# Kernel tuning notes

Hardware: AMD Instinct MI355X
Metric: run time of the kernel (lower is better)

## Reference

```python
import jax, jax.numpy as jnp
import numpy as np

N_NODES = 100000
N_EDGES = 1600000
NUM_GRAPHS = 256


def _gcn_conv(x, src, dst, deg_isqrt, deg_inv, W, b):
    # GCNConv with self-loops and symmetric normalization (PyG semantics):
    # out_i = sum_{j->i} d_j^-1/2 d_i^-1/2 (x_j W) + d_i^-1 (x_i W) + b
    xl = x @ W  # [N, out]
    norm = deg_isqrt[src] * deg_isqrt[dst]  # [E]
    msgs = norm[:, None] * xl[src]  # [E, out] -- dominant memory traffic
    agg = jax.ops.segment_sum(msgs, dst, num_segments=N_NODES)
    return agg + deg_inv[:, None] * xl + b


def setup_inputs() -> dict:
    key = jax.random.key(0)
    ks = jax.random.split(key, 8)
    F_in, H, T = 128, 128, 64
    x = jax.random.normal(ks[0], (N_NODES, F_in), dtype=jnp.float32)
    edge_index = jax.random.randint(ks[1], (2, N_EDGES), 0, N_NODES, dtype=jnp.int64)
    batch = jnp.sort(jax.random.randint(ks[2], (N_NODES,), 0, NUM_GRAPHS, dtype=jnp.int64))
    s0 = 1.0 / np.sqrt(F_in)
    s1 = 1.0 / np.sqrt(H)
    return {
        "x": x,
        "edge_index": edge_index,
        "batch": batch,
        "W0": jax.random.normal(ks[3], (F_in, H), dtype=jnp.float32) * s0,
        "b0": jnp.zeros((H,), dtype=jnp.float32),
        "W1": jax.random.normal(ks[4], (H, H), dtype=jnp.float32) * s1,
        "b1": jnp.zeros((H,), dtype=jnp.float32),
        "W2": jax.random.normal(ks[5], (H, T), dtype=jnp.float32) * s1,
        "b2": jnp.zeros((T,), dtype=jnp.float32),
    }


def reference(x, edge_index, batch, W0, b0, W1, b1, W2, b2):
    src, dst = edge_index[0], edge_index[1]
    # degree including self-loop
    deg = jax.ops.segment_sum(jnp.ones((N_EDGES,), x.dtype), dst, num_segments=N_NODES) + 1.0
    deg_isqrt = jax.lax.rsqrt(deg)
    deg_inv = 1.0 / deg

    h = jax.nn.gelu(_gcn_conv(x, src, dst, deg_isqrt, deg_inv, W0, b0))
    h = jax.nn.gelu(_gcn_conv(h, src, dst, deg_isqrt, deg_inv, W1, b1))
    h = jax.nn.gelu(_gcn_conv(h, src, dst, deg_isqrt, deg_inv, W2, b2))

    # global_mean_pool over graphs
    sums = jax.ops.segment_sum(h, batch, num_segments=NUM_GRAPHS)
    counts = jax.ops.segment_sum(jnp.ones((N_NODES,), h.dtype), batch, num_segments=NUM_GRAPHS)
    return sums / jnp.maximum(counts, 1.0)[:, None]
```

## Files before the change

### kernel.cpp

```cpp
#include <hip/hip_runtime.h>
#include <math.h>

#define F_IN 128
#define TDIM 64
#define NGRAPH 256

typedef __attribute__((ext_vector_type(8))) short short8;
typedef __attribute__((ext_vector_type(4))) float f32x4;

__device__ __forceinline__ float gelu_f(float x) {
    float x3 = x * x * x;
    return 0.5f * x * (1.0f + tanhf(0.7978845608028654f * (x + 0.044715f * x3)));
}

__device__ __forceinline__ unsigned short bf16_of(float x) {
    unsigned u = __float_as_uint(x);
    return (unsigned short)((u + 0x7fffu + ((u >> 16) & 1u)) >> 16);
}
__device__ __forceinline__ float f_of(unsigned short h) {
    return __uint_as_float(((unsigned)h) << 16);
}
__device__ __forceinline__ unsigned bf16pair(float a, float b) {
    return (unsigned)bf16_of(a) | ((unsigned)bf16_of(b) << 16);
}
__device__ __forceinline__ float2 bf16unpack(unsigned u) {
    float2 r;
    r.x = __uint_as_float(u << 16);
    r.y = __uint_as_float(u & 0xffff0000u);
    return r;
}


#define BIN_CH 4096
#define MAXNB 512
#define CAP 6144

__global__ __launch_bounds__(256) void binC_kernel(const int* __restrict__ src,
                                                   const int* __restrict__ dst,
                                                   int* __restrict__ bucket_cnt,
                                                   unsigned* __restrict__ tmp, int E, int NB) {
    __shared__ int hist[MAXNB];
    __shared__ int hbase[MAXNB];
    __shared__ int hcur[MAXNB];
    int tid = threadIdx.x;
    int base = blockIdx.x * BIN_CH;
    int end = base + BIN_CH;
    if (end > E) end = E;
    for (int i = tid; i < NB; i += 256) hist[i] = 0;
    __syncthreads();
    for (int e = base + tid; e < end; e += 256) atomicAdd(&hist[dst[e] >> 8], 1);
    __syncthreads();
    for (int i = tid; i < NB; i += 256) {
        int c = hist[i];
        hbase[i] = (c > 0) ? atomicAdd(&bucket_cnt[i], c) : 0;
        hcur[i] = 0;
    }
    __syncthreads();
    for (int e = base + tid; e < end; e += 256) {
        int d = dst[e];
        int b = d >> 8;
        int p = atomicAdd(&hcur[b], 1);
        int slot = hbase[b] + p;
        if (slot < CAP)
            tmp[(size_t)b * CAP + slot] = (unsigned)src[e] | ((unsigned)(d & 255) << 24);
    }
}

__global__ void scanBuckets_kernel(const int* __restrict__ bucket_cnt,
                                   int* __restrict__ bbase, int* __restrict__ row_off,
                                   int NB, int N) {
    if (threadIdx.x == 0 && blockIdx.x == 0) {
        int c = 0;
        for (int i = 0; i < NB; ++i) {
            bbase[i] = c;
            int v = bucket_cnt[i];
            c += (v < CAP ? v : CAP);
        }
        row_off[N] = c;
    }
}

__global__ __launch_bounds__(256) void binDcount_kernel(const unsigned* __restrict__ tmp,
                                                        const int* __restrict__ bucket_cnt,
                                                        const int* __restrict__ bbase,
                                                        int* __restrict__ row_off,
                                                        float* __restrict__ isq,
                                                        float* __restrict__ dinv, int N) {
    __shared__ int lcnt[256];
    __shared__ int sh[256];
    int b = blockIdx.x;
    int tid = threadIdx.x;
    int cntb = bucket_cnt[b];
    if (cntb > CAP) cntb = CAP;
    lcnt[tid] = 0;
    __syncthreads();
    const unsigned* tb = tmp + (size_t)b * CAP;
    for (int e = tid; e < cntb; e += 256) atomicAdd(&lcnt[tb[e] >> 24], 1);
    __syncthreads();
    int own = lcnt[tid];
    sh[tid] = own;
    __syncthreads();
    for (int off = 1; off < 256; off <<= 1) {
        int x = (tid >= off) ? sh[tid - off] : 0;
        __syncthreads();
        sh[tid] += x;
        __syncthreads();
    }
    int excl = sh[tid] - own;
    int node = (b << 8) + tid;
    if (node < N) {
        row_off[node] = bbase[b] + excl;
        float d = (float)own + 1.0f;
        isq[node] = rsqrtf(d);
        dinv[node] = 1.0f / d;
    }
}

__global__ __launch_bounds__(256) void binDscatter_kernel(const unsigned* __restrict__ tmp,
                                                          const int* __restrict__ bucket_cnt,
                                                          const int* __restrict__ row_off,
                                                          const float* __restrict__ isq,
                                                          uint2* __restrict__ edges, int N) {
    __shared__ int lcur[256];
    __shared__ float lisq[256];
    int b = blockIdx.x;
    int node0 = b << 8;
    int tid = threadIdx.x;
    lcur[tid] = 0;
    int nd = node0 + tid;
    lisq[tid] = (nd < N) ? isq[nd] : 0.f;
    __syncthreads();
    int cntb = bucket_cnt[b];
    if (cntb > CAP) cntb = CAP;
    const unsigned* tb = tmp + (size_t)b * CAP;
    for (int e = tid; e < cntb; e += 256) {
        unsigned rec = tb[e];
        int dl = (int)(rec >> 24);
        unsigned s = rec & 0xFFFFFFu;
        int p = atomicAdd(&lcur[dl], 1);
        float nrm = isq[s] * lisq[dl];
        edges[(size_t)row_off[node0 + dl] + p] = make_uint2(s, __float_as_uint(nrm));
    }
}


__global__ __launch_bounds__(256) void wconv_all_kernel(const float* __restrict__ W0,
                                                        const float* __restrict__ W1,
                                                        const float* __restrict__ W2,
                                                        unsigned short* __restrict__ hi0,
                                                        unsigned short* __restrict__ lo0,
                                                        unsigned short* __restrict__ hi1,
                                                        unsigned short* __restrict__ lo1,
                                                        unsigned short* __restrict__ hi2,
                                                        unsigned short* __restrict__ lo2) {
    int idx = blockIdx.x * blockDim.x + threadIdx.x;
    const float* W;
    unsigned short *whi, *wlo;
    int local, FOUT;
    if (idx < 16384) {
        W = W0; whi = hi0; wlo = lo0; local = idx; FOUT = 128;
    } else if (idx < 32768) {
        W = W1; whi = hi1; wlo = lo1; local = idx - 16384; FOUT = 128;
    } else if (idx < 40960) {
        W = W2; whi = hi2; wlo = lo2; local = idx - 32768; FOUT = 64;
    } else {
        return;
    }
    int k = local / FOUT;
    int n = local % FOUT;
    float w = W[local];
    unsigned short h = bf16_of(w);
    whi[(size_t)n * 128 + k] = h;
    wlo[(size_t)n * 128 + k] = bf16_of(w - f_of(h));
}


#define LROW 136

template <int FOUT>
__global__ __launch_bounds__(256) void gemm_mfma_kernel(const float* __restrict__ X,
                                                        const unsigned short* __restrict__ whiT,
                                                        const unsigned short* __restrict__ wloT,
                                                        unsigned* __restrict__ Yb, int nrows) {
    constexpr int NT = FOUT / 16;
    __shared__ short lds[2 * FOUT * LROW];
    short* shi = lds;
    short* slo = lds + FOUT * LROW;

    for (int c = threadIdx.x; c < FOUT * 16; c += 256) {
        int n = c >> 4, r = c & 15;
        *(short8*)(shi + n * LROW + r * 8) = *(const short8*)(whiT + (size_t)n * 128 + r * 8);
        *(short8*)(slo + n * LROW + r * 8) = *(const short8*)(wloT + (size_t)n * 128 + r * 8);
    }
    __syncthreads();

    int lane = threadIdx.x & 63;
    int wave = threadIdx.x >> 6;
    int quad = lane >> 4;
    int l16 = lane & 15;
    int rowBase = blockIdx.x * 128 + wave * 32;

    f32x4 acc[2][NT];
#pragma unroll
    for (int m = 0; m < 2; ++m)
#pragma unroll
        for (int t = 0; t < NT; ++t) acc[m][t] = (f32x4){0.f, 0.f, 0.f, 0.f};

    int arow0 = rowBase + l16;
    int arow1 = rowBase + 16 + l16;
    bool ok0 = arow0 < nrows, ok1 = arow1 < nrows;
    const float* xr0 = X + (size_t)arow0 * 128;
    const float* xr1 = X + (size_t)arow1 * 128;

#pragma unroll
    for (int k0 = 0; k0 < 128; k0 += 32) {
        short8 ahi[2], alo[2];
#pragma unroll
        for (int m = 0; m < 2; ++m) {
            const float* xr = m ? xr1 : xr0;
            bool ok = m ? ok1 : ok0;
            float xv[8];
            if (ok) {
                float4 v0 = *(const float4*)(xr + k0 + quad * 8);
                float4 v1 = *(const float4*)(xr + k0 + quad * 8 + 4);
                xv[0] = v0.x; xv[1] = v0.y; xv[2] = v0.z; xv[3] = v0.w;
                xv[4] = v1.x; xv[5] = v1.y; xv[6] = v1.z; xv[7] = v1.w;
            } else {
#pragma unroll
                for (int j = 0; j < 8; ++j) xv[j] = 0.f;
            }
#pragma unroll
            for (int j = 0; j < 8; ++j) {
                unsigned short h = bf16_of(xv[j]);
                ahi[m][j] = (short)h;
                alo[m][j] = (short)bf16_of(xv[j] - f_of(h));
            }
        }
#pragma unroll
        for (int t = 0; t < NT; ++t) {
            int off = (t * 16 + l16) * LROW + k0 + quad * 8;
            short8 bhi = *(const short8*)(shi + off);
            short8 blo = *(const short8*)(slo + off);
#pragma unroll
            for (int m = 0; m < 2; ++m) {
                acc[m][t] = __builtin_amdgcn_mfma_f32_16x16x32_bf16(ahi[m], bhi, acc[m][t], 0, 0, 0);
                acc[m][t] = __builtin_amdgcn_mfma_f32_16x16x32_bf16(alo[m], bhi, acc[m][t], 0, 0, 0);
                acc[m][t] = __builtin_amdgcn_mfma_f32_16x16x32_bf16(ahi[m], blo, acc[m][t], 0, 0, 0);
            }
        }
    }

#pragma unroll
    for (int m = 0; m < 2; ++m) {
#pragma unroll
        for (int t = 0; t < NT; ++t) {
            int col = t * 16 + l16;
#pragma unroll
            for (int i = 0; i < 4; ++i) {
                int r = rowBase + m * 16 + quad * 4 + i;
                float v = acc[m][t][i];
                float nb = __shfl_xor(v, 1, 64);
                if (((lane & 1) == 0) && r < nrows)
                    Yb[(size_t)r * (FOUT / 2) + (col >> 1)] = bf16pair(v, nb);
            }
        }
    }
}


__global__ __launch_bounds__(256) void agg128_kernel(const unsigned* __restrict__ xlb,
                                                     const int* __restrict__ row_off,
                                                     const uint2* __restrict__ edges,
                                                     const float* __restrict__ dinv,
                                                     const float* __restrict__ bias,
                                                     float* __restrict__ out, int nnodes) {
    int wave = (blockIdx.x * blockDim.x + threadIdx.x) >> 6;
    int lane = threadIdx.x & 63;
    if (wave >= nnodes) return;
    int e0 = __builtin_amdgcn_readfirstlane(row_off[wave]);
    int e1 = __builtin_amdgcn_readfirstlane(row_off[wave + 1]);
    float ax = 0.f, ay = 0.f;
    int rounds = (e1 - e0 + 15) >> 4;
    for (int r = 0; r < rounds; ++r) {
        int base = e0 + (r << 4);
        int idx = base + (lane & 15);
        int cl = idx < e1 ? idx : e1 - 1;
        uint2 edv = edges[cl];
        unsigned sx[16];
        float nw[16];
#pragma unroll
        for (int j = 0; j < 16; ++j) {
            sx[j] = (unsigned)__builtin_amdgcn_readlane((int)edv.x, j);
            unsigned ny = (unsigned)__builtin_amdgcn_readlane((int)edv.y, j);
            nw[j] = (base + j < e1) ? __uint_as_float(ny) : 0.f;
        }
        unsigned v[16];
#pragma unroll
        for (int j = 0; j < 16; ++j) v[j] = xlb[(size_t)sx[j] * 64 + lane];
#pragma unroll
        for (int j = 0; j < 16; ++j) {
            float2 f = bf16unpack(v[j]);
            ax += nw[j] * f.x;
            ay += nw[j] * f.y;
        }
    }
    float di = dinv[wave];
    float2 pi = bf16unpack(xlb[(size_t)wave * 64 + lane]);
    float2 bb = *(const float2*)(bias + lane * 2);
    float2 o;
    o.x = gelu_f(ax + di * pi.x + bb.x);
    o.y = gelu_f(ay + di * pi.y + bb.y);
    *(float2*)(out + (size_t)wave * 128 + lane * 2) = o;
}


__global__ __launch_bounds__(256) void agg64_kernel(const unsigned* __restrict__ xlb,
                                                    const int* __restrict__ row_off,
                                                    const uint2* __restrict__ edges,
                                                    const float* __restrict__ dinv,
                                                    const float* __restrict__ bias,
                                                    float* __restrict__ out, int nnodes) {
    int wave = (blockIdx.x * blockDim.x + threadIdx.x) >> 6;
    int lane = threadIdx.x & 63;
    int sub = lane >> 5;
    int sl = lane & 31;
    int node = wave * 2 + sub;
    bool nv = node < nnodes;
    int e0 = nv ? row_off[node] : 0;
    int e1 = nv ? row_off[node + 1] : 0;
    int rounds = (e1 - e0 + 15) >> 4;
    int ro = __shfl_xor(rounds, 32, 64);
    int maxr = rounds > ro ? rounds : ro;
    float ax = 0.f, ay = 0.f;
    for (int r = 0; r < maxr; ++r) {
        int base = e0 + (r << 4);
        uint2 ed[16];
#pragma unroll
        for (int j = 0; j < 16; ++j) {
            int idx = base + j;
            int cl = idx < e1 ? idx : (e1 > e0 ? e1 - 1 : 0);
            ed[j] = edges[cl];
            if (idx >= e1) ed[j].y = 0u;
        }
        unsigned v[16];
#pragma unroll
        for (int j = 0; j < 16; ++j) v[j] = xlb[(size_t)ed[j].x * 32 + sl];
#pragma unroll
        for (int j = 0; j < 16; ++j) {
            float nw = __uint_as_float(ed[j].y);
            float2 f = bf16unpack(v[j]);
            ax += nw * f.x;
            ay += nw * f.y;
        }
    }
    if (nv) {
        float di = dinv[node];
        float2 pi = bf16unpack(xlb[(size_t)node * 32 + sl]);
        float2 bb = *(const float2*)(bias + sl * 2);
        float2 o;
        o.x = gelu_f(ax + di * pi.x + bb.x);
        o.y = gelu_f(ay + di * pi.y + bb.y);
        *(float2*)(out + (size_t)node * 64 + sl * 2) = o;
    }
}


#define POOL_CHUNK 64

__global__ __launch_bounds__(256) void pool_kernel(const float* __restrict__ h,
                                                   const int* __restrict__ batch,
                                                   float* __restrict__ psum,
                                                   float* __restrict__ pcnt, int nnodes) {
    int wave = (blockIdx.x * blockDim.x + threadIdx.x) >> 6;
    int lane = threadIdx.x & 63;
    int n0 = wave * POOL_CHUNK;
    if (n0 >= nnodes) return;
    int n1 = n0 + POOL_CHUNK;
    if (n1 > nnodes) n1 = nnodes;

    int g_cur = batch[n0];
    float acc = 0.f;
    int cnt = 0;
    for (int node = n0; node < n1; ++node) {
        int g = batch[node];
        if (g != g_cur) {
            atomicAdd(&psum[g_cur * TDIM + lane], acc);
            if (lane == 0) atomicAdd(&pcnt[g_cur], (float)cnt);
            acc = 0.f;
            cnt = 0;
            g_cur = g;
        }
        acc += h[(size_t)node * TDIM + lane];
        ++cnt;
    }
    atomicAdd(&psum[g_cur * TDIM + lane], acc);
    if (lane == 0) atomicAdd(&pcnt[g_cur], (float)cnt);
}

__global__ __launch_bounds__(256) void fin_kernel(const float* __restrict__ psum,
                                                  const float* __restrict__ pcnt,
                                                  float* __restrict__ out) {
    int i = blockIdx.x * blockDim.x + threadIdx.x;
    if (i < NGRAPH * TDIM) {
        float c = pcnt[i >> 6];
        out[i] = psum[i] / fmaxf(c, 1.0f);
    }
}


extern "C" void kernel_launch(void* const* d_in, const int* in_sizes, int n_in,
                              void* d_out, int out_size, void* d_ws, size_t ws_size,
                              hipStream_t stream) {
    const float* x = (const float*)d_in[0];
    const int* ei = (const int*)d_in[1];
    const int* batch = (const int*)d_in[2];
    const float* W0 = (const float*)d_in[3];
    const float* b0 = (const float*)d_in[4];
    const float* W1 = (const float*)d_in[5];
    const float* b1 = (const float*)d_in[6];
    const float* W2 = (const float*)d_in[7];
    const float* b2 = (const float*)d_in[8];

    const int N = in_sizes[0] / F_IN;
    const int E = in_sizes[1] / 2;
    const int* src = ei;
    const int* dst = ei + E;
    const int NB = (N + 255) >> 8;

    char* w = (char*)d_ws;
    auto alloc = [&](size_t bytes) -> void* {
        void* p = (void*)w;
        w += (bytes + 255) & ~(size_t)255;
        return p;
    };
    float* isq = (float*)alloc((size_t)N * 4);
    float* dinv = (float*)alloc((size_t)N * 4);
    int* bucket_cnt = (int*)alloc((size_t)MAXNB * 4);
    int* bbase = (int*)alloc((size_t)MAXNB * 4);
    int* row_off = (int*)alloc((size_t)(N + 1) * 4);
    uint2* edges = (uint2*)alloc((size_t)E * 8);
    unsigned* tmp = (unsigned*)alloc((size_t)NB * CAP * 4);
    float* psum = (float*)alloc((size_t)NGRAPH * TDIM * 4);
    float* pcnt = (float*)alloc((size_t)NGRAPH * 4);
    float* bufH = (float*)alloc((size_t)N * 128 * 4);
    unsigned* bufXb = (unsigned*)alloc((size_t)N * 64 * 4);
    unsigned short* whiT0 = (unsigned short*)alloc(128 * 128 * 2);
    unsigned short* wloT0 = (unsigned short*)alloc(128 * 128 * 2);
    unsigned short* whiT1 = (unsigned short*)alloc(128 * 128 * 2);
    unsigned short* wloT1 = (unsigned short*)alloc(128 * 128 * 2);
    unsigned short* whiT2 = (unsigned short*)alloc(64 * 128 * 2);
    unsigned short* wloT2 = (unsigned short*)alloc(64 * 128 * 2);

    hipMemsetAsync(bucket_cnt, 0, (size_t)MAXNB * 4, stream);
    hipMemsetAsync(psum, 0, (size_t)NGRAPH * TDIM * 4, stream);
    hipMemsetAsync(pcnt, 0, (size_t)NGRAPH * 4, stream);

    int cblocks = (E + BIN_CH - 1) / BIN_CH;
    binC_kernel<<<cblocks, 256, 0, stream>>>(src, dst, bucket_cnt, tmp, E, NB);
    scanBuckets_kernel<<<1, 64, 0, stream>>>(bucket_cnt, bbase, row_off, NB, N);
    binDcount_kernel<<<NB, 256, 0, stream>>>(tmp, bucket_cnt, bbase, row_off, isq, dinv, N);
    binDscatter_kernel<<<NB, 256, 0, stream>>>(tmp, bucket_cnt, row_off, isq, edges, N);

    wconv_all_kernel<<<(40960 + 255) / 256, 256, 0, stream>>>(W0, W1, W2, whiT0, wloT0, whiT1,
                                                              wloT1, whiT2, wloT2);

    int gblocks = (N + 127) / 128;
    int ablocks = (N * 64 + 255) / 256;
    int a64blocks = (((N + 1) / 2) * 64 + 255) / 256;

    gemm_mfma_kernel<128><<<gblocks, 256, 0, stream>>>(x, whiT0, wloT0, bufXb, N);
    agg128_kernel<<<ablocks, 256, 0, stream>>>(bufXb, row_off, edges, dinv, b0, bufH, N);
    gemm_mfma_kernel<128><<<gblocks, 256, 0, stream>>>(bufH, whiT1, wloT1, bufXb, N);
    agg128_kernel<<<ablocks, 256, 0, stream>>>(bufXb, row_off, edges, dinv, b1, bufH, N);
    gemm_mfma_kernel<64><<<gblocks, 256, 0, stream>>>(bufH, whiT2, wloT2, bufXb, N);
    agg64_kernel<<<a64blocks, 256, 0, stream>>>(bufXb, row_off, edges, dinv, b2, bufH, N);

    int pwaves = (N + POOL_CHUNK - 1) / POOL_CHUNK;
    int pblocks = (pwaves * 64 + 255) / 256;
    pool_kernel<<<pblocks, 256, 0, stream>>>(bufH, batch, psum, pcnt, N);
    fin_kernel<<<(NGRAPH * TDIM + 255) / 256, 256, 0, stream>>>(psum, pcnt, (float*)d_out);
}
```

Baseline: 458.6 us.

## Store hidden activations in bf16 and merge scan with weight conversion

The aggregation kernels now write post-GELU activations as packed bf16 instead of fp32. The layer-2/3 GEMMs read those bf16 activations directly as single MFMA A operands, and the pooling kernel unpacks bf16. The goal is to halve activation write/read traffic between layers and to drop one kernel launch by folding weight conversion into the bucket scan kernel. In exchange, intermediate activations lose precision, since only the hi/lo split of the weights is kept.

```diff
diff --git a/kernel.cpp b/kernel.cpp
--- a/kernel.cpp
+++ b/kernel.cpp
@@ -66,18 +66,49 @@
     }
 }
 
-__global__ void scanBuckets_kernel(const int* __restrict__ bucket_cnt,
-                                   int* __restrict__ bbase, int* __restrict__ row_off,
-                                   int NB, int N) {
-    if (threadIdx.x == 0 && blockIdx.x == 0) {
-        int c = 0;
-        for (int i = 0; i < NB; ++i) {
-            bbase[i] = c;
-            int v = bucket_cnt[i];
-            c += (v < CAP ? v : CAP);
-        }
-        row_off[N] = c;
-    }
+__global__ __launch_bounds__(256) void scan_wconv_kernel(const int* __restrict__ bucket_cnt,
+                                                         int* __restrict__ bbase,
+                                                         int* __restrict__ row_off, int NB,
+                                                         int N, const float* __restrict__ W0,
+                                                         const float* __restrict__ W1,
+                                                         const float* __restrict__ W2,
+                                                         unsigned short* __restrict__ hi0,
+                                                         unsigned short* __restrict__ lo0,
+                                                         unsigned short* __restrict__ hi1,
+                                                         unsigned short* __restrict__ lo1,
+                                                         unsigned short* __restrict__ hi2,
+                                                         unsigned short* __restrict__ lo2) {
+    if (blockIdx.x == 0) {
+        if (threadIdx.x == 0) {
+            int c = 0;
+            for (int i = 0; i < NB; ++i) {
+                bbase[i] = c;
+                int v = bucket_cnt[i];
+                c += (v < CAP ? v : CAP);
+            }
+            row_off[N] = c;
+        }
+        return;
+    }
+    int idx = (blockIdx.x - 1) * 256 + threadIdx.x;
+    const float* W;
+    unsigned short *whi, *wlo;
+    int local, FOUT;
+    if (idx < 16384) {
+        W = W0; whi = hi0; wlo = lo0; local = idx; FOUT = 128;
+    } else if (idx < 32768) {
+        W = W1; whi = hi1; wlo = lo1; local = idx - 16384; FOUT = 128;
+    } else if (idx < 40960) {
+        W = W2; whi = hi2; wlo = lo2; local = idx - 32768; FOUT = 64;
+    } else {
+        return;
+    }
+    int k = local / FOUT;
+    int n = local % FOUT;
+    float w = W[local];
+    unsigned short h = bf16_of(w);
+    whi[(size_t)n * 128 + k] = h;
+    wlo[(size_t)n * 128 + k] = bf16_of(w - f_of(h));
 }
 
 __global__ __launch_bounds__(256) void binDcount_kernel(const unsigned* __restrict__ tmp,
@@ -144,44 +175,13 @@
 }
 
 
-__global__ __launch_bounds__(256) void wconv_all_kernel(const float* __restrict__ W0,
-                                                        const float* __restrict__ W1,
-                                                        const float* __restrict__ W2,
-                                                        unsigned short* __restrict__ hi0,
-                                                        unsigned short* __restrict__ lo0,
-                                                        unsigned short* __restrict__ hi1,
-                                                        unsigned short* __restrict__ lo1,
-                                                        unsigned short* __restrict__ hi2,
-                                                        unsigned short* __restrict__ lo2) {
-    int idx = blockIdx.x * blockDim.x + threadIdx.x;
-    const float* W;
-    unsigned short *whi, *wlo;
-    int local, FOUT;
-    if (idx < 16384) {
-        W = W0; whi = hi0; wlo = lo0; local = idx; FOUT = 128;
-    } else if (idx < 32768) {
-        W = W1; whi = hi1; wlo = lo1; local = idx - 16384; FOUT = 128;
-    } else if (idx < 40960) {
-        W = W2; whi = hi2; wlo = lo2; local = idx - 32768; FOUT = 64;
-    } else {
-        return;
-    }
-    int k = local / FOUT;
-    int n = local % FOUT;
-    float w = W[local];
-    unsigned short h = bf16_of(w);
-    whi[(size_t)n * 128 + k] = h;
-    wlo[(size_t)n * 128 + k] = bf16_of(w - f_of(h));
-}
-
-
 #define LROW 136
 
-template <int FOUT>
-__global__ __launch_bounds__(256) void gemm_mfma_kernel(const float* __restrict__ X,
-                                                        const unsigned short* __restrict__ whiT,
-                                                        const unsigned short* __restrict__ wloT,
-                                                        unsigned* __restrict__ Yb, int nrows) {
+__global__ __launch_bounds__(256) void gemm_f32_kernel(const float* __restrict__ X,
+                                                       const unsigned short* __restrict__ whiT,
+                                                       const unsigned short* __restrict__ wloT,
+                                                       unsigned* __restrict__ Yb, int nrows) {
+    constexpr int FOUT = 128;
     constexpr int NT = FOUT / 16;
     __shared__ short lds[2 * FOUT * LROW];
     short* shi = lds;
@@ -268,12 +268,90 @@
 }
 
 
+template <int FOUT>
+__global__ __launch_bounds__(256) void gemm_bf16_kernel(const unsigned* __restrict__ Xb,
+                                                        const unsigned short* __restrict__ whiT,
+                                                        const unsigned short* __restrict__ wloT,
+                                                        unsigned* __restrict__ Yb, int nrows) {
+    constexpr int NT = FOUT / 16;
+    __shared__ short lds[2 * FOUT * LROW];
+    short* shi = lds;
+    short* slo = lds + FOUT * LROW;
+
+    for (int c = threadIdx.x; c < FOUT * 16; c += 256) {
+        int n = c >> 4, r = c & 15;
+        *(short8*)(shi + n * LROW + r * 8) = *(const short8*)(whiT + (size_t)n * 128 + r * 8);
+        *(short8*)(slo + n * LROW + r * 8) = *(const short8*)(wloT + (size_t)n * 128 + r * 8);
+    }
+    __syncthreads();
+
+    int lane = threadIdx.x & 63;
+    int wave = threadIdx.x >> 6;
+    int quad = lane >> 4;
+    int l16 = lane & 15;
+    int rowBase = blockIdx.x * 128 + wave * 32;
+
+    f32x4 acc[2][NT];
+#pragma unroll
+    for (int m = 0; m < 2; ++m)
+#pragma unroll
+        for (int t = 0; t < NT; ++t) acc[m][t] = (f32x4){0.f, 0.f, 0.f, 0.f};
+
+    int arow0 = rowBase + l16;
+    int arow1 = rowBase + 16 + l16;
+    bool ok0 = arow0 < nrows, ok1 = arow1 < nrows;
+    const short* xs0 = (const short*)Xb + (size_t)arow0 * 128;
+    const short* xs1 = (const short*)Xb + (size_t)arow1 * 128;
+
+#pragma unroll
+    for (int k0 = 0; k0 < 128; k0 += 32) {
+        short8 a[2];
+#pragma unroll
+        for (int m = 0; m < 2; ++m) {
+            const short* xs = m ? xs1 : xs0;
+            bool ok = m ? ok1 : ok0;
+            if (ok)
+                a[m] = *(const short8*)(xs + k0 + quad * 8);
+            else
+                a[m] = (short8){0, 0, 0, 0, 0, 0, 0, 0};
+        }
+#pragma unroll
+        for (int t = 0; t < NT; ++t) {
+            int off = (t * 16 + l16) * LROW + k0 + quad * 8;
+            short8 bhi = *(const short8*)(shi + off);
+            short8 blo = *(const short8*)(slo + off);
+#pragma unroll
+            for (int m = 0; m < 2; ++m) {
+                acc[m][t] = __builtin_amdgcn_mfma_f32_16x16x32_bf16(a[m], bhi, acc[m][t], 0, 0, 0);
+                acc[m][t] = __builtin_amdgcn_mfma_f32_16x16x32_bf16(a[m], blo, acc[m][t], 0, 0, 0);
+            }
+        }
+    }
+
+#pragma unroll
+    for (int m = 0; m < 2; ++m) {
+#pragma unroll
+        for (int t = 0; t < NT; ++t) {
+            int col = t * 16 + l16;
+#pragma unroll
+            for (int i = 0; i < 4; ++i) {
+                int r = rowBase + m * 16 + quad * 4 + i;
+                float v = acc[m][t][i];
+                float nb = __shfl_xor(v, 1, 64);
+                if (((lane & 1) == 0) && r < nrows)
+                    Yb[(size_t)r * (FOUT / 2) + (col >> 1)] = bf16pair(v, nb);
+            }
+        }
+    }
+}
+
+
 __global__ __launch_bounds__(256) void agg128_kernel(const unsigned* __restrict__ xlb,
                                                      const int* __restrict__ row_off,
                                                      const uint2* __restrict__ edges,
                                                      const float* __restrict__ dinv,
                                                      const float* __restrict__ bias,
-                                                     float* __restrict__ out, int nnodes) {
+                                                     unsigned* __restrict__ outb, int nnodes) {
     int wave = (blockIdx.x * blockDim.x + threadIdx.x) >> 6;
     int lane = threadIdx.x & 63;
     if (wave >= nnodes) return;
@@ -307,10 +385,8 @@
     float di = dinv[wave];
     float2 pi = bf16unpack(xlb[(size_t)wave * 64 + lane]);
     float2 bb = *(const float2*)(bias + lane * 2);
-    float2 o;
-    o.x = gelu_f(ax + di * pi.x + bb.x);
-    o.y = gelu_f(ay + di * pi.y + bb.y);
-    *(float2*)(out + (size_t)wave * 128 + lane * 2) = o;
+    outb[(size_t)wave * 64 + lane] =
+        bf16pair(gelu_f(ax + di * pi.x + bb.x), gelu_f(ay + di * pi.y + bb.y));
 }
 
 
@@ -319,7 +395,7 @@
                                                     const uint2* __restrict__ edges,
                                                     const float* __restrict__ dinv,
                                                     const float* __restrict__ bias,
-                                                    float* __restrict__ out, int nnodes) {
+                                                    unsigned* __restrict__ outb, int nnodes) {
     int wave = (blockIdx.x * blockDim.x + threadIdx.x) >> 6;
     int lane = threadIdx.x & 63;
     int sub = lane >> 5;
@@ -357,44 +433,49 @@
         float di = dinv[node];
         float2 pi = bf16unpack(xlb[(size_t)node * 32 + sl]);
         float2 bb = *(const float2*)(bias + sl * 2);
-        float2 o;
-        o.x = gelu_f(ax + di * pi.x + bb.x);
-        o.y = gelu_f(ay + di * pi.y + bb.y);
-        *(float2*)(out + (size_t)node * 64 + sl * 2) = o;
+        outb[(size_t)node * 32 + sl] =
+            bf16pair(gelu_f(ax + di * pi.x + bb.x), gelu_f(ay + di * pi.y + bb.y));
     }
 }
 
 
 #define POOL_CHUNK 64
 
-__global__ __launch_bounds__(256) void pool_kernel(const float* __restrict__ h,
+__global__ __launch_bounds__(256) void pool_kernel(const unsigned* __restrict__ hb,
                                                    const int* __restrict__ batch,
                                                    float* __restrict__ psum,
                                                    float* __restrict__ pcnt, int nnodes) {
     int wave = (blockIdx.x * blockDim.x + threadIdx.x) >> 6;
     int lane = threadIdx.x & 63;
-    int n0 = wave * POOL_CHUNK;
+    int half = lane >> 5;
+    int p = lane & 31;
+    int n0 = wave * POOL_CHUNK + half * 32;
     if (n0 >= nnodes) return;
-    int n1 = n0 + POOL_CHUNK;
+    int n1 = n0 + 32;
     if (n1 > nnodes) n1 = nnodes;
 
     int g_cur = batch[n0];
-    float acc = 0.f;
+    float accx = 0.f, accy = 0.f;
     int cnt = 0;
     for (int node = n0; node < n1; ++node) {
         int g = batch[node];
         if (g != g_cur) {
-            atomicAdd(&psum[g_cur * TDIM + lane], acc);
-            if (lane == 0) atomicAdd(&pcnt[g_cur], (float)cnt);
-            acc = 0.f;
+            atomicAdd(&psum[g_cur * TDIM + 2 * p], accx);
+            atomicAdd(&psum[g_cur * TDIM + 2 * p + 1], accy);
+            if (p == 0) atomicAdd(&pcnt[g_cur], (float)cnt);
+            accx = 0.f;
+            accy = 0.f;
             cnt = 0;
             g_cur = g;
         }
-        acc += h[(size_t)node * TDIM + lane];
+        float2 f = bf16unpack(hb[(size_t)node * 32 + p]);
+        accx += f.x;
+        accy += f.y;
         ++cnt;
     }
-    atomicAdd(&psum[g_cur * TDIM + lane], acc);
-    if (lane == 0) atomicAdd(&pcnt[g_cur], (float)cnt);
+    atomicAdd(&psum[g_cur * TDIM + 2 * p], accx);
+    atomicAdd(&psum[g_cur * TDIM + 2 * p + 1], accy);
+    if (p == 0) atomicAdd(&pcnt[g_cur], (float)cnt);
 }
 
 __global__ __launch_bounds__(256) void fin_kernel(const float* __restrict__ psum,
@@ -442,8 +523,8 @@
     unsigned* tmp = (unsigned*)alloc((size_t)NB * CAP * 4);
     float* psum = (float*)alloc((size_t)NGRAPH * TDIM * 4);
     float* pcnt = (float*)alloc((size_t)NGRAPH * 4);
-    float* bufH = (float*)alloc((size_t)N * 128 * 4);
     unsigned* bufXb = (unsigned*)alloc((size_t)N * 64 * 4);
+    unsigned* bufHb = (unsigned*)alloc((size_t)N * 64 * 4);
     unsigned short* whiT0 = (unsigned short*)alloc(128 * 128 * 2);
     unsigned short* wloT0 = (unsigned short*)alloc(128 * 128 * 2);
     unsigned short* whiT1 = (unsigned short*)alloc(128 * 128 * 2);
@@ -457,26 +538,25 @@
 
     int cblocks = (E + BIN_CH - 1) / BIN_CH;
     binC_kernel<<<cblocks, 256, 0, stream>>>(src, dst, bucket_cnt, tmp, E, NB);
-    scanBuckets_kernel<<<1, 64, 0, stream>>>(bucket_cnt, bbase, row_off, NB, N);
+    scan_wconv_kernel<<<1 + (40960 + 255) / 256, 256, 0, stream>>>(
+        bucket_cnt, bbase, row_off, NB, N, W0, W1, W2, whiT0, wloT0, whiT1, wloT1, whiT2,
+        wloT2);
     binDcount_kernel<<<NB, 256, 0, stream>>>(tmp, bucket_cnt, bbase, row_off, isq, dinv, N);
     binDscatter_kernel<<<NB, 256, 0, stream>>>(tmp, bucket_cnt, row_off, isq, edges, N);
-
-    wconv_all_kernel<<<(40960 + 255) / 256, 256, 0, stream>>>(W0, W1, W2, whiT0, wloT0, whiT1,
-                                                              wloT1, whiT2, wloT2);
 
     int gblocks = (N + 127) / 128;
     int ablocks = (N * 64 + 255) / 256;
     int a64blocks = (((N + 1) / 2) * 64 + 255) / 256;
 
-    gemm_mfma_kernel<128><<<gblocks, 256, 0, stream>>>(x, whiT0, wloT0, bufXb, N);
-    agg128_kernel<<<ablocks, 256, 0, stream>>>(bufXb, row_off, edges, dinv, b0, bufH, N);
-    gemm_mfma_kernel<128><<<gblocks, 256, 0, stream>>>(bufH, whiT1, wloT1, bufXb, N);
-    agg128_kernel<<<ablocks, 256, 0, stream>>>(bufXb, row_off, edges, dinv, b1, bufH, N);
-    gemm_mfma_kernel<64><<<gblocks, 256, 0, stream>>>(bufH, whiT2, wloT2, bufXb, N);
-    agg64_kernel<<<a64blocks, 256, 0, stream>>>(bufXb, row_off, edges, dinv, b2, bufH, N);
+    gemm_f32_kernel<<<gblocks, 256, 0, stream>>>(x, whiT0, wloT0, bufXb, N);
+    agg128_kernel<<<ablocks, 256, 0, stream>>>(bufXb, row_off, edges, dinv, b0, bufHb, N);
+    gemm_bf16_kernel<128><<<gblocks, 256, 0, stream>>>(bufHb, whiT1, wloT1, bufXb, N);
+    agg128_kernel<<<ablocks, 256, 0, stream>>>(bufXb, row_off, edges, dinv, b1, bufHb, N);
+    gemm_bf16_kernel<64><<<gblocks, 256, 0, stream>>>(bufHb, whiT2, wloT2, bufXb, N);
+    agg64_kernel<<<a64blocks, 256, 0, stream>>>(bufXb, row_off, edges, dinv, b2, bufHb, N);
 
     int pwaves = (N + POOL_CHUNK - 1) / POOL_CHUNK;
     int pblocks = (pwaves * 64 + 255) / 256;
-    pool_kernel<<<pblocks, 256, 0, stream>>>(bufH, batch, psum, pcnt, N);
+    pool_kernel<<<pblocks, 256, 0, stream>>>(bufHb, batch, psum, pcnt, N);
     fin_kernel<<<(NGRAPH * TDIM + 255) / 256, 256, 0, stream>>>(psum, pcnt, (float*)d_out);
 }
```

After: 435.8 us. -5.0%, faster.
